# Optimization experiments

Hardware: AMD Instinct MI355X
Metric: run time of the kernel (lower is better)

The kernel has to match this reference:

```python
import jax, jax.numpy as jnp
import numpy as np


def setup_inputs() -> dict:
    key = jax.random.key(0)
    x = jax.random.normal(key, (16, 64, 512, 512), dtype=jnp.float32)
    return {"x": x}


def reference(x) -> jnp.ndarray:
    # PartialDerivative with dim=0: diagonal (c,c,2,1) kernel with weights
    # [-1, +1] along H == forward finite difference along the H axis.
    # out[b,c,h,w] = x[b,c,h+1,w] - x[b,c,h,w], shape (b, c, h-1, w)
    return x[:, :, 1:, :] - x[:, :, :-1, :]
```

## Files before the change

### kernel.cpp

```cpp
#include <hip/hip_runtime.h>


#define H_IN 512
#define H_OUT 511
#define W4 128
#define PLANE_OUT (H_OUT * W4)
#define PLANE_IN  (H_IN * W4)

__global__ __launch_bounds__(256) void PartialDerivative_kernel(
    const float4* __restrict__ x, float4* __restrict__ out) {
    const int tid = blockIdx.x * blockDim.x + threadIdx.x;
    if (tid >= PLANE_OUT) return;
    const int bc = blockIdx.y;

    const size_t in_base = (size_t)bc * PLANE_IN + (size_t)tid;
    float4 a = x[in_base];
    float4 b = x[in_base + W4];
    float4 r;
    r.x = b.x - a.x;
    r.y = b.y - a.y;
    r.z = b.z - a.z;
    r.w = b.w - a.w;
    out[(size_t)bc * PLANE_OUT + (size_t)tid] = r;
}

extern "C" void kernel_launch(void* const* d_in, const int* in_sizes, int n_in,
                              void* d_out, int out_size, void* d_ws, size_t ws_size,
                              hipStream_t stream) {
    const float4* x = (const float4*)d_in[0];
    float4* out = (float4*)d_out;

    dim3 block(256);
    dim3 grid((PLANE_OUT + 255) / 256, 16 * 64);
    PartialDerivative_kernel<<<grid, block, 0, stream>>>(x, out);
}
```

Before: 373.6 us.

## Stream rows per thread with register reuse and nontemporal stores

Each thread now walks a chunk of 64 rows down the H axis for one float4 column. It keeps the previous row in a register, so every input row is loaded once instead of twice. Outputs are written with nontemporal stores so they do not pollute the cache. The cost is fewer threads and a serial loop per thread, which leaves less memory-level parallelism than the flat one-element-per-thread launch.

```diff
diff --git a/kernel.cpp b/kernel.cpp
--- a/kernel.cpp
+++ b/kernel.cpp
@@ -1,36 +1,44 @@
 #include <hip/hip_runtime.h>
 
 
-#define H_IN 512
-#define H_OUT 511
-#define W4 128
-#define PLANE_OUT (H_OUT * W4)
-#define PLANE_IN  (H_IN * W4)
+typedef float f32x4 __attribute__((ext_vector_type(4)));
+
+#define H_IN   512
+#define H_OUT  511
+#define W4     128
+#define CHUNKS 8
+#define CH_H   64
 
 __global__ __launch_bounds__(256) void PartialDerivative_kernel(
-    const float4* __restrict__ x, float4* __restrict__ out) {
-    const int tid = blockIdx.x * blockDim.x + threadIdx.x;
-    if (tid >= PLANE_OUT) return;
-    const int bc = blockIdx.y;
+    const f32x4* __restrict__ x, f32x4* __restrict__ out) {
+    const int t  = blockIdx.x * 256 + threadIdx.x;
+    const int w4 = t & (W4 - 1);
+    const int ck = (t >> 7) & (CHUNKS - 1);
+    const int bc = t >> 10;
 
-    const size_t in_base = (size_t)bc * PLANE_IN + (size_t)tid;
-    float4 a = x[in_base];
-    float4 b = x[in_base + W4];
-    float4 r;
-    r.x = b.x - a.x;
-    r.y = b.y - a.y;
-    r.z = b.z - a.z;
-    r.w = b.w - a.w;
-    out[(size_t)bc * PLANE_OUT + (size_t)tid] = r;
+    const int h0   = ck * CH_H;
+    const int nout = (ck == CHUNKS - 1) ? (CH_H - 1) : CH_H;
+
+    const f32x4* xp = x   + (size_t)bc * (H_IN * W4)  + (size_t)h0 * W4 + w4;
+    f32x4*       op = out + (size_t)bc * (H_OUT * W4) + (size_t)h0 * W4 + w4;
+
+    f32x4 prev = xp[0];
+    #pragma unroll 4
+    for (int i = 0; i < nout; ++i) {
+        f32x4 nxt = xp[(size_t)(i + 1) * W4];
+        f32x4 r = nxt - prev;
+        __builtin_nontemporal_store(r, &op[(size_t)i * W4]);
+        prev = nxt;
+    }
 }
 
 extern "C" void kernel_launch(void* const* d_in, const int* in_sizes, int n_in,
                               void* d_out, int out_size, void* d_ws, size_t ws_size,
                               hipStream_t stream) {
-    const float4* x = (const float4*)d_in[0];
-    float4* out = (float4*)d_out;
+    const f32x4* x = (const f32x4*)d_in[0];
+    f32x4* out = (f32x4*)d_out;
 
     dim3 block(256);
-    dim3 grid((PLANE_OUT + 255) / 256, 16 * 64);
+    dim3 grid((16 * 64 * CHUNKS * W4) / 256);
     PartialDerivative_kernel<<<grid, block, 0, stream>>>(x, out);
 }
```

After: 430.7 us. +15.3%, slower.
